# Performance work log

Hardware: AMD Instinct MI355X
Metric: run time of the kernel (lower is better)

Reference implementation:

```python
import jax, jax.numpy as jnp
import numpy as np

B, N = 2, 4096
IN_CH, OUT_CH = 64, 64
L_MAX, NR = 3, 4
KERNEL_RADIUS = 0.5
PATCH = 64  # hardcoded in torch topk(-dist, 64)


def setup_inputs() -> dict:
    key = jax.random.key(0)
    k1, k2, k3 = jax.random.split(key, 3)
    xyz = jax.random.normal(k1, (B, N, 3), dtype=jnp.float32)
    signal = jax.random.normal(k2, (B, N, IN_CH), dtype=jnp.float32)
    # xavier_uniform on (out, in, nr, l_max+1): receptive = nr*(l_max+1)
    recept = NR * (L_MAX + 1)
    bound = float(np.sqrt(6.0 / (IN_CH * recept + OUT_CH * recept)))
    weight = jax.random.uniform(k3, (OUT_CH, IN_CH, NR, L_MAX + 1), dtype=jnp.float32,
                                minval=-bound, maxval=bound)
    biases = jnp.zeros((OUT_CH,), dtype=jnp.float32)
    return {"xyz": xyz, "signal": signal, "weight": weight, "biases": biases}


def _sph(X):
    # X: [B,N,P,3] l2-normalized patch directions -> [B,N,P,(L_MAX+1)^2]
    x, y, z = X[..., 0], X[..., 1], X[..., 2]
    x2, y2, z2 = x * x, y * y, z * z
    Ys = []
    Ys.append(jnp.full_like(x, 0.5 * np.sqrt(1.0 / np.pi)))           # Y00
    s3 = np.sqrt(3.0 / np.pi) / 2.0
    Ys += [s3 * y, s3 * z, -s3 * x]                                    # l=1
    s15h = np.sqrt(15.0 / np.pi) / 2.0
    s15q = np.sqrt(15.0 / np.pi) / 4.0
    s5q = np.sqrt(5.0 / np.pi) / 4.0
    Ys += [s15h * x * y, s15h * y * z, s5q * (2.0 * z2 - x2 - y2),
           -s15h * z * x, s15q * (x2 - y2)]                            # l=2
    c33 = np.sqrt(35.0 / (2.0 * np.pi)) / 4.0
    c32 = np.sqrt(105.0 / np.pi) / 2.0
    c31 = np.sqrt(21.0 / (2.0 * np.pi)) / 4.0
    c30 = np.sqrt(7.0 / np.pi) / 4.0
    c32b = np.sqrt(105.0 / np.pi) / 4.0
    Ys += [c33 * (3.0 * x2 * y - y * y2),
           c32 * x * y * z,
           c31 * (4.0 * y * z2 - x2 * y - y * y2),
           c30 * (2.0 * z * z2 - 3.0 * x2 * z - 3.0 * y2 * z),
           -c31 * (4.0 * z2 * x - x * x2 - x * y2),
           c32b * (x2 * z - y2 * z),
           -c33 * (x * x2 - 3.0 * x * y2)]                             # l=3
    return jnp.stack(Ys, axis=-1)


def reference(xyz, signal, weight, biases):
    # pairwise squared distances via matmul (costly_cdist)
    r2 = jnp.sum(xyz * xyz, axis=2)                                    # [B,N]
    sqd = r2[:, :, None] - 2.0 * jnp.einsum('bnd,bmd->bnm', xyz, xyz) + r2[:, None, :]
    neg_vals, idx = jax.lax.top_k(-sqd, PATCH)                         # KNN
    sq_patches_dist = -neg_vals                                        # [B,N,P]
    gather = jax.vmap(lambda pts, i: pts[i])                           # per-batch fancy gather
    patches = gather(xyz, idx) - xyz[:, :, None, :]                    # [B,N,P,3]
    # F.normalize(p=2, dim=-1, eps=0.01): x / max(||x||, eps)
    nrm = jnp.linalg.norm(patches, axis=-1, keepdims=True)
    Y = _sph(patches / jnp.maximum(nrm, 0.01))                         # [B,N,P,K2]
    dist = jnp.sqrt(jnp.maximum(sq_patches_dist, 1e-4))                # [B,N,P]
    r_grid = jnp.linspace(0.0, KERNEL_RADIUS, NR, dtype=jnp.float32)   # [NR]
    sigma = KERNEL_RADIUS / (NR - 1)
    rad = jnp.exp(-jnp.square(dist[..., None] - r_grid) / (2.0 * sigma ** 2))  # [B,N,P,NR]
    yk = Y[:, :, :, None, :] * rad[..., None]                          # [B,N,P,NR,K2]
    y_w = jnp.sum(yk[:, :, :, 0, 0], axis=2)[:, :, None, None, None]   # [B,N,1,1,1]
    conv_kernel = yk / (y_w + 1e-6)
    sig_patches = gather(signal, idx)                                  # [B,N,P,C]
    y = jnp.einsum('bvprn,bvpc->bvcrn', conv_kernel, sig_patches)
    y = y * y
    bands = [jnp.sum(y[..., l * l:(l + 1) * (l + 1)], axis=-1) for l in range(L_MAX + 1)]
    y = jnp.stack(bands, axis=-1)                                      # [B,N,C,NR,L+1]
    y = jnp.sqrt(jnp.maximum(y, 1e-4))
    out = jnp.einsum('ijrn,bvjrn->bvi', weight, y) + biases
    return out
```

## Files before the change

### kernel.cpp

```cpp
#include <hip/hip_runtime.h>
#include <hip/hip_bf16.h>
#include <math.h>

#define NB 2
#define NPTS 4096
#define CH 64
#define PATCH 64

typedef __attribute__((ext_vector_type(8))) short s16x8;
typedef __attribute__((ext_vector_type(4))) short s16x4;
typedef __attribute__((ext_vector_type(4))) float f32x4;
typedef __attribute__((ext_vector_type(4))) unsigned u32x4;

static __device__ __forceinline__ short f2bf(float f) {
    union { __hip_bfloat16 h; short s; } u;
    u.h = __float2bfloat16(f);
    return u.s;
}

__global__ __launch_bounds__(256) void prep_kernel(const float* __restrict__ W,
                                                   short* __restrict__ Wfrag,
                                                   const float* __restrict__ xyz,
                                                   float4* __restrict__ xyz4,
                                                   const float* __restrict__ signal,
                                                   unsigned short* __restrict__ sigbf) {
    const int bid = blockIdx.x;
    const int tid = threadIdx.x;
    if (bid < 32) {
        const int gid = bid * 256 + tid;
        const int mt = gid >> 11;
        const int st = (gid >> 6) & 31;
        const int l  = gid & 63;
        const int i  = mt * 16 + (l & 15);
        const int k0 = st * 32 + (l >> 4) * 8;
        const f32x4 a = *(const f32x4*)&W[i * 1024 + k0];
        const f32x4 c = *(const f32x4*)&W[i * 1024 + k0 + 4];
        s16x8 v;
        v[0] = f2bf(a[0]); v[1] = f2bf(a[1]); v[2] = f2bf(a[2]); v[3] = f2bf(a[3]);
        v[4] = f2bf(c[0]); v[5] = f2bf(c[1]); v[6] = f2bf(c[2]); v[7] = f2bf(c[3]);
        *(s16x8*)&Wfrag[gid * 8] = v;
    } else if (bid < 64) {
        const int idx = (bid - 32) * 256 + tid;
        const float x = xyz[idx * 3 + 0];
        const float y = xyz[idx * 3 + 1];
        const float z = xyz[idx * 3 + 2];
        float4 v;
        v.x = x; v.y = y; v.z = z;
        v.w = fmaf(x, x, fmaf(y, y, z * z));
        xyz4[idx] = v;
    } else {
        const int g = (bid - 64) * 256 + tid;
        const size_t base = (size_t)g * 32;
#pragma unroll
        for (int u = 0; u < 8; ++u) {
            const f32x4 v = *(const f32x4*)&signal[base + u * 4];
            s16x4 o;
            o[0] = f2bf(v[0]); o[1] = f2bf(v[1]); o[2] = f2bf(v[2]); o[3] = f2bf(v[3]);
            *(s16x4*)&sigbf[base + u * 4] = o;
        }
    }
}

__global__ __launch_bounds__(256, 8) void knn_kernel(const float4* __restrict__ xyz4,
                                                     int* __restrict__ knn_idx) {
    const int pt   = blockIdx.x;
    const int b    = pt >> 12;
    const int q    = pt & (NPTS - 1);
    const int tid  = threadIdx.x;
    const int wv   = tid >> 6;
    const int lane = tid & 63;

    __shared__ __align__(16) unsigned hist[2048];
    __shared__ __align__(16) unsigned short sbin[4096];
    __shared__ unsigned wsum[4];
    __shared__ unsigned sh_H;
    __shared__ int sh_need;
    __shared__ int cnt_less, cnt_tie;

    const float4* xb = xyz4 + (size_t)b * NPTS;
    const float4 qp = xb[q];

#pragma unroll
    for (int u = 0; u < 2; ++u)
        ((u32x4*)hist)[u * 256 + tid] = (u32x4){0u, 0u, 0u, 0u};
    if (tid == 0) { cnt_less = 0; cnt_tie = 0; }
    __syncthreads();

#pragma unroll 4
    for (int i = 0; i < 16; ++i) {
        const int m = i * 256 + tid;
        const float4 p = xb[m];
        const float dx = p.x - qp.x;
        const float dy = p.y - qp.y;
        const float dz = p.z - qp.z;
        const float sq = fmaf(dx, dx, fmaf(dy, dy, dz * dz));
        const unsigned hk = __float_as_uint(sq) >> 19;
        sbin[i * 256 + tid] = (unsigned short)hk;
        atomicAdd(&hist[hk & 2047], 1u << ((hk >> 11) << 4));
    }
    __syncthreads();

    const int wb2 = (tid & 127) * 16;
    const int shp = (tid >> 7) << 4;
    unsigned tsum = 0;
#pragma unroll
    for (int u = 0; u < 4; ++u) {
        const u32x4 h4 = *(const u32x4*)&hist[wb2 + u * 4];
        tsum += ((h4[0] >> shp) & 0xFFFFu) + ((h4[1] >> shp) & 0xFFFFu)
              + ((h4[2] >> shp) & 0xFFFFu) + ((h4[3] >> shp) & 0xFFFFu);
    }
    unsigned run = tsum;
#pragma unroll
    for (int off = 1; off < 64; off <<= 1) {
        const unsigned v = __shfl_up(run, off);
        if (lane >= off) run += v;
    }
    if (lane == 63) wsum[wv] = run;
    __syncthreads();
    unsigned wbase = 0;
    for (int w2 = 0; w2 < wv; ++w2) wbase += wsum[w2];
    const unsigned incl = wbase + run;
    const unsigned excl = incl - tsum;
    if ((int)excl < PATCH && PATCH <= (int)incl) {
        int nrem = PATCH - (int)excl;
        for (int u = 0; u < 16; ++u) {
            const unsigned cb = (hist[wb2 + u] >> shp) & 0xFFFFu;
            if (nrem <= (int)cb) { sh_H = (unsigned)(tid * 16 + u); sh_need = nrem; break; }
            nrem -= (int)cb;
        }
    }
    __syncthreads();

    const unsigned H = sh_H;
    const int need  = sh_need;
    const int nless = PATCH - need;
    int* optr = knn_idx + (size_t)pt * PATCH;
    unsigned* ckey = hist;
    unsigned* cidx = hist + 1024;

#pragma unroll 4
    for (int i = 0; i < 16; ++i) {
        const int m = i * 256 + tid;
        const unsigned hk = sbin[i * 256 + tid];
        if (hk < H) {
            const int pos = atomicAdd(&cnt_less, 1);
            optr[pos] = m;
        } else if (hk == H) {
            const int pos = atomicAdd(&cnt_tie, 1);
            if (pos < 1024) {
                const float4 p = xb[m];
                const float dx = p.x - qp.x;
                const float dy = p.y - qp.y;
                const float dz = p.z - qp.z;
                const float sq = fmaf(dx, dx, fmaf(dy, dy, dz * dz));
                ckey[pos] = __float_as_uint(sq);
                cidx[pos] = m;
            }
        }
    }
    __syncthreads();

    const int nc = min(cnt_tie, 1024);
    for (int i = tid; i < nc; i += 256) {
        const unsigned ki = ckey[i];
        int rank = 0;
        for (int j = 0; j < nc; ++j) {
            const unsigned kj = ckey[j];
            rank += (kj < ki || (kj == ki && j < i)) ? 1 : 0;
        }
        if (rank < need) optr[nless + rank] = cidx[i];
    }
}

__global__ __launch_bounds__(256, 4) void conv_kernel(const float4* __restrict__ xyz4,
                                                      const unsigned short* __restrict__ sigbf,
                                                      const short* __restrict__ Wfrag,
                                                      const float* __restrict__ biases,
                                                      const int* __restrict__ knn_idx,
                                                      float* __restrict__ out) {
    const int tid  = threadIdx.x;
    const int wv   = tid >> 6;
    const int lane = tid & 63;
    const int ln15 = lane & 15;
    const int kq   = lane >> 4;

    __shared__ __align__(16) short cks_bf[4096];
    __shared__ __align__(16) short ckF[4096];
    __shared__ __align__(16) short sigF[4096];
    __shared__ __align__(16) short zb[4 * 1032];
    __shared__ int   sIdx4[256];
    __shared__ float sh_inv;

    sIdx4[tid] = knn_idx[(size_t)blockIdx.x * 256 + tid];
    __syncthreads();

    const int b = blockIdx.x >> 10;
    const float4* xbase = xyz4 + (size_t)b * NPTS;
    const unsigned short* sgb = sigbf + (size_t)b * NPTS * CH;

    float4 pcp, pnp;
    s16x8 pre0, pre1, pre2, pre3;

    if (wv == 0) {
        pcp = xbase[(blockIdx.x * 4) & (NPTS - 1)];
        pnp = xbase[sIdx4[lane]];
    } else if (wv <= 2) {
        const int s  = wv - 1;
        const int pb = s * 32 + kq * 8;
#pragma unroll
        for (int j = 0; j < 8; ++j) {
            const int row = sIdx4[pb + j];
            const unsigned short* rp = sgb + ((size_t)row << 6) + ln15;
            pre0[j] = (short)rp[0];
            pre1[j] = (short)rp[16];
            pre2[j] = (short)rp[32];
            pre3[j] = (short)rp[48];
        }
    }

    for (int it = 0; it < 4; ++it) {
        if (wv == 0) {
            const int p = lane;
            const float dx = pnp.x - pcp.x;
            const float dy = pnp.y - pcp.y;
            const float dz = pnp.z - pcp.z;
            const float nrm2 = dx * dx + dy * dy + dz * dz;
            const float inv_n = 1.0f / fmaxf(sqrtf(nrm2), 0.01f);
            const float x = dx * inv_n, y = dy * inv_n, z = dz * inv_n;
            const float x2 = x * x, y2 = y * y, zz = z * z;

            float Y[16];
            Y[0] = 0.28209479177387814f;
            const float s3 = 0.4886025119029199f;
            Y[1] = s3 * y;  Y[2] = s3 * z;  Y[3] = -s3 * x;
            const float s15h = 1.0925484305920792f;
            const float s15q = 0.5462742152960396f;
            const float s5q  = 0.31539156525252005f;
            Y[4] = s15h * x * y;
            Y[5] = s15h * y * z;
            Y[6] = s5q * (2.0f * zz - x2 - y2);
            Y[7] = -s15h * z * x;
            Y[8] = s15q * (x2 - y2);
            const float c33  = 0.5900435899266435f;
            const float c32  = 2.8906114426405543f;
            const float c31  = 0.4570457994644658f;
            const float c30  = 0.3731763325901154f;
            const float c32b = 1.4453057213202771f;
            Y[9]  = c33 * (3.0f * x2 * y - y * y2);
            Y[10] = c32 * x * y * z;
            Y[11] = c31 * (4.0f * y * zz - x2 * y - y * y2);
            Y[12] = c30 * (2.0f * z * zz - 3.0f * x2 * z - 3.0f * y2 * z);
            Y[13] = -c31 * (4.0f * zz * x - x * x2 - x * y2);
            Y[14] = c32b * (x2 * z - y2 * z);
            Y[15] = -c33 * (x * x2 - 3.0f * x * y2);

            const float dist = sqrtf(fmaxf(nrm2, 1e-4f));
            const float d1 = dist - 0.16666667f;
            const float d2 = dist - 0.33333334f;
            const float d3 = dist - 0.5f;
            float rad[4];
            rad[0] = expf(-dist * dist * 18.0f);
            rad[1] = expf(-d1 * d1 * 18.0f);
            rad[2] = expf(-d2 * d2 * 18.0f);
            rad[3] = expf(-d3 * d3 * 18.0f);

            const int pm = p & 15;
#pragma unroll
            for (int chunk = 0; chunk < 16; ++chunk) {
                const int r  = chunk >> 2;
                const int kb = (chunk & 3) * 4;
                s16x4 v;
                v[0] = f2bf(Y[kb + 0] * rad[r]);
                v[1] = f2bf(Y[kb + 1] * rad[r]);
                v[2] = f2bf(Y[kb + 2] * rad[r]);
                v[3] = f2bf(Y[kb + 3] * rad[r]);
                *(s16x4*)&cks_bf[p * 64 + ((chunk ^ pm) << 2)] = v;
            }
            float v = 0.28209479177387814f * rad[0];
#pragma unroll
            for (int off = 32; off > 0; off >>= 1) v += __shfl_down(v, off);
            if (p == 0) sh_inv = 1.0f / (v + 1e-6f);
        } else if (wv <= 2) {
            const int s = wv - 1;
            *(s16x8*)&sigF[(0 * 2 + s) * 512 + lane * 8] = pre0;
            *(s16x8*)&sigF[(1 * 2 + s) * 512 + lane * 8] = pre1;
            *(s16x8*)&sigF[(2 * 2 + s) * 512 + lane * 8] = pre2;
            *(s16x8*)&sigF[(3 * 2 + s) * 512 + lane * 8] = pre3;
        }
        __syncthreads();

#pragma unroll
        for (int ff = 0; ff < 2; ++ff) {
            const int f  = wv + ff * 4;
            const int mt = f >> 1, s = f & 1;
            const int rk = mt * 16 + ln15;
            const int rsw = rk >> 2, rlo = rk & 3;
            const int pb = s * 32 + kq * 8;
            s16x8 av;
#pragma unroll
            for (int j = 0; j < 8; ++j) {
                const int p = pb + j;
                av[j] = cks_bf[p * 64 + ((rsw ^ (p & 15)) << 2) + rlo];
            }
            *(s16x8*)&ckF[f * 512 + lane * 8] = av;
        }
        __syncthreads();

        if (it < 3) {
            if (wv == 0) {
                pcp = xbase[(blockIdx.x * 4 + it + 1) & (NPTS - 1)];
                pnp = xbase[sIdx4[(it + 1) * 64 + lane]];
            } else if (wv <= 2) {
                const int s  = wv - 1;
                const int pb = s * 32 + kq * 8;
#pragma unroll
                for (int j = 0; j < 8; ++j) {
                    const int row = sIdx4[(it + 1) * 64 + pb + j];
                    const unsigned short* rp = sgb + ((size_t)row << 6) + ln15;
                    pre0[j] = (short)rp[0];
                    pre1[j] = (short)rp[16];
                    pre2[j] = (short)rp[32];
                    pre3[j] = (short)rp[48];
                }
            }
        }

        const s16x8 bf0 = *(const s16x8*)&sigF[(wv * 2 + 0) * 512 + lane * 8];
        const s16x8 bf1 = *(const s16x8*)&sigF[(wv * 2 + 1) * 512 + lane * 8];
        f32x4 acc0 = {0.f, 0.f, 0.f, 0.f}, acc1 = acc0, acc2 = acc0, acc3 = acc0;
        {
            s16x8 a;
            a = *(const s16x8*)&ckF[0 * 512 + lane * 8];
            acc0 = __builtin_amdgcn_mfma_f32_16x16x32_bf16(a, bf0, acc0, 0, 0, 0);
            a = *(const s16x8*)&ckF[1 * 512 + lane * 8];
            acc0 = __builtin_amdgcn_mfma_f32_16x16x32_bf16(a, bf1, acc0, 0, 0, 0);
            a = *(const s16x8*)&ckF[2 * 512 + lane * 8];
            acc1 = __builtin_amdgcn_mfma_f32_16x16x32_bf16(a, bf0, acc1, 0, 0, 0);
            a = *(const s16x8*)&ckF[3 * 512 + lane * 8];
            acc1 = __builtin_amdgcn_mfma_f32_16x16x32_bf16(a, bf1, acc1, 0, 0, 0);
            a = *(const s16x8*)&ckF[4 * 512 + lane * 8];
            acc2 = __builtin_amdgcn_mfma_f32_16x16x32_bf16(a, bf0, acc2, 0, 0, 0);
            a = *(const s16x8*)&ckF[5 * 512 + lane * 8];
            acc2 = __builtin_amdgcn_mfma_f32_16x16x32_bf16(a, bf1, acc2, 0, 0, 0);
            a = *(const s16x8*)&ckF[6 * 512 + lane * 8];
            acc3 = __builtin_amdgcn_mfma_f32_16x16x32_bf16(a, bf0, acc3, 0, 0, 0);
            a = *(const s16x8*)&ckF[7 * 512 + lane * 8];
            acc3 = __builtin_amdgcn_mfma_f32_16x16x32_bf16(a, bf1, acc3, 0, 0, 0);
        }

        const float inv = sh_inv;
        const int qq = kq;
        float rb[4][4];
#pragma unroll
        for (int mt = 0; mt < 4; ++mt) {
            f32x4 av = (mt == 0) ? acc0 : (mt == 1) ? acc1 : (mt == 2) ? acc2 : acc3;
            const float y0 = av[0] * inv, y1 = av[1] * inv;
            const float y2 = av[2] * inv, y3 = av[3] * inv;
            const float sA = y0 * y0;
            const float sB = y1 * y1 + y2 * y2 + y3 * y3;
            const float sAll = sA + sB;
            float b0 = (qq == 0) ? sA : 0.0f;
            float b1 = (qq == 0) ? sB : 0.0f;
            float b2 = (qq == 1) ? sAll : ((qq == 2) ? sA : 0.0f);
            float b3 = (qq == 3) ? sAll : ((qq == 2) ? sB : 0.0f);
            b0 += __shfl_xor(b0, 16); b0 += __shfl_xor(b0, 32);
            b1 += __shfl_xor(b1, 16); b1 += __shfl_xor(b1, 32);
            b2 += __shfl_xor(b2, 16); b2 += __shfl_xor(b2, 32);
            b3 += __shfl_xor(b3, 16); b3 += __shfl_xor(b3, 32);
            rb[mt][0] = b0; rb[mt][1] = b1; rb[mt][2] = b2; rb[mt][3] = b3;
        }
        float s0 = rb[0][0], s1 = rb[0][1], s2 = rb[0][2], s3 = rb[0][3];
#pragma unroll
        for (int mt = 1; mt < 4; ++mt) {
            s0 = (qq == mt) ? rb[mt][0] : s0;
            s1 = (qq == mt) ? rb[mt][1] : s1;
            s2 = (qq == mt) ? rb[mt][2] : s2;
            s3 = (qq == mt) ? rb[mt][3] : s3;
        }
        s16x4 zv;
        zv[0] = f2bf(sqrtf(fmaxf(s0, 1e-4f)));
        zv[1] = f2bf(sqrtf(fmaxf(s1, 1e-4f)));
        zv[2] = f2bf(sqrtf(fmaxf(s2, 1e-4f)));
        zv[3] = f2bf(sqrtf(fmaxf(s3, 1e-4f)));
        const int c = wv * 16 + ln15;
        *(s16x4*)&zb[it * 1032 + c * 16 + qq * 4] = zv;

        if (it < 3) __syncthreads();
    }
    __syncthreads();

    const int mt5 = wv;
    const int g   = ln15 & 3;
    f32x4 acc5 = {0.f, 0.f, 0.f, 0.f};
#pragma unroll 4
    for (int st = 0; st < 32; ++st) {
        const s16x8 a  = *(const s16x8*)&Wfrag[((mt5 * 32 + st) * 64 + lane) * 8];
        const s16x8 zf = *(const s16x8*)&zb[g * 1032 + st * 32 + kq * 8];
        acc5 = __builtin_amdgcn_mfma_f32_16x16x32_bf16(a, zf, acc5, 0, 0, 0);
    }
    if (ln15 < 4) {
        const int i0 = mt5 * 16 + kq * 4;
        const int orow = (blockIdx.x * 4 + g) * CH;
#pragma unroll
        for (int rg = 0; rg < 4; ++rg)
            out[orow + i0 + rg] = acc5[rg] + biases[i0 + rg];
    }
}

extern "C" void kernel_launch(void* const* d_in, const int* in_sizes, int n_in,
                              void* d_out, int out_size, void* d_ws, size_t ws_size,
                              hipStream_t stream) {
    const float* xyz    = (const float*)d_in[0];
    const float* signal = (const float*)d_in[1];
    const float* weight = (const float*)d_in[2];
    const float* biases = (const float*)d_in[3];
    float* out = (float*)d_out;

    char* ws = (char*)d_ws;
    int*            knn_idx = (int*)ws;
    short*          Wfrag   = (short*)(ws + 0x200000);
    float4*         xyz4    = (float4*)(ws + 0x220000);
    unsigned short* sigbf   = (unsigned short*)(ws + 0x240000);

    prep_kernel<<<128, 256, 0, stream>>>(weight, Wfrag, xyz, xyz4, signal, sigbf);
    knn_kernel<<<NB * NPTS, 256, 0, stream>>>(xyz4, knn_idx);
    conv_kernel<<<(NB * NPTS) / 4, 256, 0, stream>>>(xyz4, sigbf, Wfrag, biases,
                                                     knn_idx, out);
}
```

Before: 88.19 us.

## Compute all four points' harmonics up front across waves and split gathers evenly

```diff
diff --git a/kernel.cpp b/kernel.cpp
--- a/kernel.cpp
+++ b/kernel.cpp
@@ -16,6 +16,9 @@
     union { __hip_bfloat16 h; short s; } u;
     u.h = __float2bfloat16(f);
     return u.s;
+}
+static __device__ __forceinline__ float bf2f(unsigned short v) {
+    return __uint_as_float(((unsigned)v) << 16);
 }
 
 __global__ __launch_bounds__(256) void prep_kernel(const float* __restrict__ W,
@@ -184,12 +187,13 @@
     const int ln15 = lane & 15;
     const int kq   = lane >> 4;
 
-    __shared__ __align__(16) short cks_bf[4096];
+    __shared__ __align__(16) short Y4[4 * 64 * 20];
+    __shared__ __align__(16) float rad4[4 * 64 * 4];
     __shared__ __align__(16) short ckF[4096];
     __shared__ __align__(16) short sigF[4096];
     __shared__ __align__(16) short zb[4 * 1032];
     __shared__ int   sIdx4[256];
-    __shared__ float sh_inv;
+    __shared__ float sh_inv4[4];
 
     sIdx4[tid] = knn_idx[(size_t)blockIdx.x * 256 + tid];
     __syncthreads();
@@ -198,132 +202,105 @@
     const float4* xbase = xyz4 + (size_t)b * NPTS;
     const unsigned short* sgb = sigbf + (size_t)b * NPTS * CH;
 
-    float4 pcp, pnp;
-    s16x8 pre0, pre1, pre2, pre3;
-
-    if (wv == 0) {
-        pcp = xbase[(blockIdx.x * 4) & (NPTS - 1)];
-        pnp = xbase[sIdx4[lane]];
-    } else if (wv <= 2) {
-        const int s  = wv - 1;
-        const int pb = s * 32 + kq * 8;
-#pragma unroll
-        for (int j = 0; j < 8; ++j) {
-            const int row = sIdx4[pb + j];
-            const unsigned short* rp = sgb + ((size_t)row << 6) + ln15;
-            pre0[j] = (short)rp[0];
-            pre1[j] = (short)rp[16];
-            pre2[j] = (short)rp[32];
-            pre3[j] = (short)rp[48];
-        }
-    }
+    {
+        const int q   = (blockIdx.x * 4 + wv) & (NPTS - 1);
+        const int idx = sIdx4[wv * 64 + lane];
+        const float4 cp = xbase[q];
+        const float4 np = xbase[idx];
+        const float dx = np.x - cp.x;
+        const float dy = np.y - cp.y;
+        const float dz = np.z - cp.z;
+        const float nrm2 = dx * dx + dy * dy + dz * dz;
+        const float inv_n = 1.0f / fmaxf(sqrtf(nrm2), 0.01f);
+        const float x = dx * inv_n, y = dy * inv_n, z = dz * inv_n;
+        const float x2 = x * x, y2 = y * y, zz = z * z;
+
+        float Y[16];
+        Y[0] = 0.28209479177387814f;
+        const float s3 = 0.4886025119029199f;
+        Y[1] = s3 * y;  Y[2] = s3 * z;  Y[3] = -s3 * x;
+        const float s15h = 1.0925484305920792f;
+        const float s15q = 0.5462742152960396f;
+        const float s5q  = 0.31539156525252005f;
+        Y[4] = s15h * x * y;
+        Y[5] = s15h * y * z;
+        Y[6] = s5q * (2.0f * zz - x2 - y2);
+        Y[7] = -s15h * z * x;
+        Y[8] = s15q * (x2 - y2);
+        const float c33  = 0.5900435899266435f;
+        const float c32  = 2.8906114426405543f;
+        const float c31  = 0.4570457994644658f;
+        const float c30  = 0.3731763325901154f;
+        const float c32b = 1.4453057213202771f;
+        Y[9]  = c33 * (3.0f * x2 * y - y * y2);
+        Y[10] = c32 * x * y * z;
+        Y[11] = c31 * (4.0f * y * zz - x2 * y - y * y2);
+        Y[12] = c30 * (2.0f * z * zz - 3.0f * x2 * z - 3.0f * y2 * z);
+        Y[13] = -c31 * (4.0f * zz * x - x * x2 - x * y2);
+        Y[14] = c32b * (x2 * z - y2 * z);
+        Y[15] = -c33 * (x * x2 - 3.0f * x * y2);
+
+        const float dist = sqrtf(fmaxf(nrm2, 1e-4f));
+        const float d1 = dist - 0.16666667f;
+        const float d2 = dist - 0.33333334f;
+        const float d3 = dist - 0.5f;
+        f32x4 rad;
+        rad[0] = expf(-dist * dist * 18.0f);
+        rad[1] = expf(-d1 * d1 * 18.0f);
+        rad[2] = expf(-d2 * d2 * 18.0f);
+        rad[3] = expf(-d3 * d3 * 18.0f);
+
+        const int ybase = (wv * 64 + lane) * 20;
+#pragma unroll
+        for (int k4 = 0; k4 < 4; ++k4) {
+            s16x4 v;
+            v[0] = f2bf(Y[k4 * 4 + 0]);
+            v[1] = f2bf(Y[k4 * 4 + 1]);
+            v[2] = f2bf(Y[k4 * 4 + 2]);
+            v[3] = f2bf(Y[k4 * 4 + 3]);
+            *(s16x4*)&Y4[ybase + k4 * 4] = v;
+        }
+        *(f32x4*)&rad4[(wv * 64 + lane) * 4] = rad;
+
+        float v = 0.28209479177387814f * rad[0];
+#pragma unroll
+        for (int off = 32; off > 0; off >>= 1) v += __shfl_down(v, off);
+        if (lane == 0) sh_inv4[wv] = 1.0f / (v + 1e-6f);
+    }
+    __syncthreads();
+
+    const int sgv  = wv & 1;
+    const int ctv  = wv >> 1;
 
     for (int it = 0; it < 4; ++it) {
-        if (wv == 0) {
-            const int p = lane;
-            const float dx = pnp.x - pcp.x;
-            const float dy = pnp.y - pcp.y;
-            const float dz = pnp.z - pcp.z;
-            const float nrm2 = dx * dx + dy * dy + dz * dz;
-            const float inv_n = 1.0f / fmaxf(sqrtf(nrm2), 0.01f);
-            const float x = dx * inv_n, y = dy * inv_n, z = dz * inv_n;
-            const float x2 = x * x, y2 = y * y, zz = z * z;
-
-            float Y[16];
-            Y[0] = 0.28209479177387814f;
-            const float s3 = 0.4886025119029199f;
-            Y[1] = s3 * y;  Y[2] = s3 * z;  Y[3] = -s3 * x;
-            const float s15h = 1.0925484305920792f;
-            const float s15q = 0.5462742152960396f;
-            const float s5q  = 0.31539156525252005f;
-            Y[4] = s15h * x * y;
-            Y[5] = s15h * y * z;
-            Y[6] = s5q * (2.0f * zz - x2 - y2);
-            Y[7] = -s15h * z * x;
-            Y[8] = s15q * (x2 - y2);
-            const float c33  = 0.5900435899266435f;
-            const float c32  = 2.8906114426405543f;
-            const float c31  = 0.4570457994644658f;
-            const float c30  = 0.3731763325901154f;
-            const float c32b = 1.4453057213202771f;
-            Y[9]  = c33 * (3.0f * x2 * y - y * y2);
-            Y[10] = c32 * x * y * z;
-            Y[11] = c31 * (4.0f * y * zz - x2 * y - y * y2);
-            Y[12] = c30 * (2.0f * z * zz - 3.0f * x2 * z - 3.0f * y2 * z);
-            Y[13] = -c31 * (4.0f * zz * x - x * x2 - x * y2);
-            Y[14] = c32b * (x2 * z - y2 * z);
-            Y[15] = -c33 * (x * x2 - 3.0f * x * y2);
-
-            const float dist = sqrtf(fmaxf(nrm2, 1e-4f));
-            const float d1 = dist - 0.16666667f;
-            const float d2 = dist - 0.33333334f;
-            const float d3 = dist - 0.5f;
-            float rad[4];
-            rad[0] = expf(-dist * dist * 18.0f);
-            rad[1] = expf(-d1 * d1 * 18.0f);
-            rad[2] = expf(-d2 * d2 * 18.0f);
-            rad[3] = expf(-d3 * d3 * 18.0f);
-
-            const int pm = p & 15;
-#pragma unroll
-            for (int chunk = 0; chunk < 16; ++chunk) {
-                const int r  = chunk >> 2;
-                const int kb = (chunk & 3) * 4;
-                s16x4 v;
-                v[0] = f2bf(Y[kb + 0] * rad[r]);
-                v[1] = f2bf(Y[kb + 1] * rad[r]);
-                v[2] = f2bf(Y[kb + 2] * rad[r]);
-                v[3] = f2bf(Y[kb + 3] * rad[r]);
-                *(s16x4*)&cks_bf[p * 64 + ((chunk ^ pm) << 2)] = v;
+        {
+            s16x8 g0, g1;
+#pragma unroll
+            for (int j = 0; j < 8; ++j) {
+                const int row = sIdx4[it * 64 + sgv * 32 + kq * 8 + j];
+                const unsigned short* rp = sgb + ((size_t)row << 6) + ctv * 16 + ln15;
+                g0[j] = (short)rp[0];
+                g1[j] = (short)rp[32];
             }
-            float v = 0.28209479177387814f * rad[0];
-#pragma unroll
-            for (int off = 32; off > 0; off >>= 1) v += __shfl_down(v, off);
-            if (p == 0) sh_inv = 1.0f / (v + 1e-6f);
-        } else if (wv <= 2) {
-            const int s = wv - 1;
-            *(s16x8*)&sigF[(0 * 2 + s) * 512 + lane * 8] = pre0;
-            *(s16x8*)&sigF[(1 * 2 + s) * 512 + lane * 8] = pre1;
-            *(s16x8*)&sigF[(2 * 2 + s) * 512 + lane * 8] = pre2;
-            *(s16x8*)&sigF[(3 * 2 + s) * 512 + lane * 8] = pre3;
-        }
-        __syncthreads();
-
+            *(s16x8*)&sigF[(ctv * 2 + sgv) * 512 + lane * 8] = g0;
+            *(s16x8*)&sigF[((ctv + 2) * 2 + sgv) * 512 + lane * 8] = g1;
+        }
 #pragma unroll
         for (int ff = 0; ff < 2; ++ff) {
             const int f  = wv + ff * 4;
             const int mt = f >> 1, s = f & 1;
-            const int rk = mt * 16 + ln15;
-            const int rsw = rk >> 2, rlo = rk & 3;
             const int pb = s * 32 + kq * 8;
             s16x8 av;
 #pragma unroll
             for (int j = 0; j < 8; ++j) {
                 const int p = pb + j;
-                av[j] = cks_bf[p * 64 + ((rsw ^ (p & 15)) << 2) + rlo];
+                const float Yv = bf2f((unsigned short)Y4[(it * 64 + p) * 20 + ln15]);
+                const float rv = rad4[(it * 64 + p) * 4 + mt];
+                av[j] = f2bf(Yv * rv);
             }
             *(s16x8*)&ckF[f * 512 + lane * 8] = av;
         }
         __syncthreads();
-
-        if (it < 3) {
-            if (wv == 0) {
-                pcp = xbase[(blockIdx.x * 4 + it + 1) & (NPTS - 1)];
-                pnp = xbase[sIdx4[(it + 1) * 64 + lane]];
-            } else if (wv <= 2) {
-                const int s  = wv - 1;
-                const int pb = s * 32 + kq * 8;
-#pragma unroll
-                for (int j = 0; j < 8; ++j) {
-                    const int row = sIdx4[(it + 1) * 64 + pb + j];
-                    const unsigned short* rp = sgb + ((size_t)row << 6) + ln15;
-                    pre0[j] = (short)rp[0];
-                    pre1[j] = (short)rp[16];
-                    pre2[j] = (short)rp[32];
-                    pre3[j] = (short)rp[48];
-                }
-            }
-        }
 
         const s16x8 bf0 = *(const s16x8*)&sigF[(wv * 2 + 0) * 512 + lane * 8];
         const s16x8 bf1 = *(const s16x8*)&sigF[(wv * 2 + 1) * 512 + lane * 8];
@@ -348,7 +325,7 @@
             acc3 = __builtin_amdgcn_mfma_f32_16x16x32_bf16(a, bf1, acc3, 0, 0, 0);
         }
 
-        const float inv = sh_inv;
+        const float inv = sh_inv4[it];
         const int qq = kq;
         float rb[4][4];
 #pragma unroll
```

Result: faster. 83.76 us (median of 2 runs) (-5.0%).
